# Performance work log

Hardware: AMD Instinct MI355X
Metric: run time of the kernel (lower is better)

The kernel has to match this reference:

```python
import jax, jax.numpy as jnp
import numpy as np

N, D, E = 100000, 128, 1600000


def setup_inputs() -> dict:
    key = jax.random.key(0)
    k1, k2, k3, k4, k5 = jax.random.split(key, 5)
    x = jax.random.normal(k1, (N, D), dtype=jnp.float32)
    edge_index = jax.random.randint(k2, (2, E), 0, N, dtype=jnp.int64)
    # xavier_uniform bound for [D, D]: sqrt(6/(D+D))
    bound = float(np.sqrt(6.0 / (D + D)))
    W_gcn = jax.random.uniform(k3, (D, D), jnp.float32, -bound, bound)
    b_gcn = jnp.zeros((D,), jnp.float32)  # GCNConv bias (default init zeros)
    # nn.Linear(bias=False) default init: uniform(-1/sqrt(fan_in), +)
    lb = float(1.0 / np.sqrt(D))
    W_ln = jax.random.uniform(k4, (D, D), jnp.float32, -lb, lb)  # [out, in]
    return {"x": x, "edge_index": edge_index, "W_gcn": W_gcn, "b_gcn": b_gcn, "W_ln": W_ln}


def gcn_conv(x, edge_index, W, b):
    n = x.shape[0]
    # add self loops
    loops = jnp.arange(n, dtype=edge_index.dtype)
    src = jnp.concatenate([edge_index[0], loops])
    dst = jnp.concatenate([edge_index[1], loops])
    h = x @ W  # [N, D] transform first (cheap), then propagate
    ones = jnp.ones(src.shape[0], dtype=x.dtype)
    deg = jax.ops.segment_sum(ones, dst, num_segments=n)  # >= 1 due to self loops
    dinv = jax.lax.rsqrt(deg)
    norm = dinv[src] * dinv[dst]  # [E+N]
    msgs = h[src] * norm[:, None]  # gather + scale
    agg = jax.ops.segment_sum(msgs, dst, num_segments=n)  # scatter-add
    return agg + b


def reference(x, edge_index, W_gcn, b_gcn, W_ln):
    out = gcn_conv(x, edge_index, W_gcn, b_gcn)
    out = jax.nn.relu(out)
    out = out @ W_ln.T  # Linear(bias=False): y = x W^T
    out = out + x       # residual
    return jax.nn.relu(out)
```

## Files before the change

kernel.cpp:

```cpp
#include <hip/hip_runtime.h>

#define DFEAT 128
#define CAP   32
#define PSH   9
#define PNODES (1 << PSH)
#define PMAX  1024
#define REGCAP 10240
#define SPILLMAX 4096
#define CHUNK 4096

__device__ __forceinline__ unsigned pack_bf16_2(float a, float b) {
    unsigned ua = __float_as_uint(a);
    unsigned ub = __float_as_uint(b);
    ua = (ua + 0x7FFFu + ((ua >> 16) & 1u)) >> 16;
    ub = (ub + 0x7FFFu + ((ub >> 16) & 1u)) >> 16;
    return ua | (ub << 16);
}

__global__ __launch_bounds__(256) void partA_kernel(const int* __restrict__ ei,
                                                    unsigned* __restrict__ rec,
                                                    int* __restrict__ gcur,
                                                    int2* __restrict__ spill,
                                                    int* __restrict__ spillcnt,
                                                    int E) {
    __shared__ int lhist[PMAX];
    int tid  = threadIdx.x;
    int base = blockIdx.x * CHUNK;
    int end  = min(base + CHUNK, E);
    for (int i = tid; i < PMAX; i += 256) lhist[i] = 0;
    __syncthreads();
    for (int e = base + tid; e < end; e += 256) {
        int dst = ei[E + e];
        atomicAdd(&lhist[dst >> PSH], 1);
    }
    __syncthreads();
    for (int p = tid; p < PMAX; p += 256) {
        int c = lhist[p];
        if (c > 0) lhist[p] = atomicAdd(&gcur[p], c);
    }
    __syncthreads();
    for (int e = base + tid; e < end; e += 256) {
        int src = ei[e];
        int dst = ei[E + e];
        int p   = dst >> PSH;
        int off = atomicAdd(&lhist[p], 1);
        if (off < REGCAP) {
            rec[(size_t)p * REGCAP + off] =
                ((unsigned)(dst & (PNODES - 1)) << 23) | (unsigned)src;
        } else {
            int sp = atomicAdd(spillcnt, 1);
            if (sp < SPILLMAX) spill[sp] = make_int2(dst, src);
        }
    }
}

__global__ __launch_bounds__(256) void partB_kernel(const unsigned* __restrict__ rec,
                                                    const int* __restrict__ gcur,
                                                    int* __restrict__ buf,
                                                    int* __restrict__ cnt,
                                                    float* __restrict__ dinv,
                                                    int2* __restrict__ spill,
                                                    int* __restrict__ spillcnt,
                                                    int n) {
    __shared__ int lcnt[PNODES];
    __shared__ int lbuf[PNODES * CAP];
    int tid   = threadIdx.x;
    int p     = blockIdx.x;
    int node0 = p << PSH;
    for (int i = tid; i < PNODES; i += 256) lcnt[i] = 0;
    __syncthreads();
    int total = gcur[p];
    if (total > REGCAP) total = REGCAP;
    const unsigned* r = rec + (size_t)p * REGCAP;
    for (int i = tid; i < total; i += 256) {
        unsigned v = r[i];
        int ldst = (int)(v >> 23);
        int src  = (int)(v & 0x7FFFFFu);
        int pos  = atomicAdd(&lcnt[ldst], 1);
        if (pos < CAP) lbuf[(ldst << 5) + pos] = src;
        else {
            int sp = atomicAdd(spillcnt, 1);
            if (sp < SPILLMAX) spill[sp] = make_int2(node0 + ldst, src);
        }
    }
    __syncthreads();
    int nn = min(PNODES, n - node0);
    if (nn <= 0) return;
    int vecs = (nn * CAP) >> 2;
    int4*       gb = (int4*)(buf + (size_t)node0 * CAP);
    const int4* lb = (const int4*)lbuf;
    for (int i = tid; i < vecs; i += 256) gb[i] = lb[i];
    for (int t = tid; t < nn; t += 256) {
        int c = lcnt[t];
        cnt[node0 + t]  = c;
        dinv[node0 + t] = rsqrtf((float)(c + 1));
    }
}

__global__ __launch_bounds__(512) void gemm1_kernel(const float* __restrict__ x,
                                                    const float* __restrict__ W,
                                                    const float* __restrict__ dinv,
                                                    unsigned* __restrict__ h, int n) {
    __shared__ float Wl[DFEAT * DFEAT];
    int tid = threadIdx.x;
#pragma unroll
    for (int it = 0; it < 8; ++it) {
        int idx = tid * 4 + it * 2048;
        *(float4*)(&Wl[idx]) = *(const float4*)(W + idx);
    }
    __syncthreads();

    int ty = tid >> 4;
    int tx = tid & 15;
    int row0 = blockIdx.x * 128 + ty * 4;
    int c0a = tx * 4, c0b = 64 + tx * 4;

    int rr[4];
#pragma unroll
    for (int i = 0; i < 4; i++) { int r = row0 + i; rr[i] = (r < n) ? r : (n - 1); }

    float acc[4][8];
#pragma unroll
    for (int i = 0; i < 4; i++)
#pragma unroll
        for (int j = 0; j < 8; j++) acc[i][j] = 0.f;

    for (int k = 0; k < DFEAT; k += 4) {
        float4 a[4];
#pragma unroll
        for (int i = 0; i < 4; i++)
            a[i] = *(const float4*)(x + (size_t)rr[i] * DFEAT + k);
#pragma unroll
        for (int kk = 0; kk < 4; kk++) {
            float4 w0 = *(const float4*)(&Wl[(k + kk) * DFEAT + c0a]);
            float4 w1 = *(const float4*)(&Wl[(k + kk) * DFEAT + c0b]);
#pragma unroll
            for (int i = 0; i < 4; i++) {
                float av = (kk == 0) ? a[i].x : (kk == 1) ? a[i].y : (kk == 2) ? a[i].z : a[i].w;
                acc[i][0] = fmaf(av, w0.x, acc[i][0]);
                acc[i][1] = fmaf(av, w0.y, acc[i][1]);
                acc[i][2] = fmaf(av, w0.z, acc[i][2]);
                acc[i][3] = fmaf(av, w0.w, acc[i][3]);
                acc[i][4] = fmaf(av, w1.x, acc[i][4]);
                acc[i][5] = fmaf(av, w1.y, acc[i][5]);
                acc[i][6] = fmaf(av, w1.z, acc[i][6]);
                acc[i][7] = fmaf(av, w1.w, acc[i][7]);
            }
        }
    }
#pragma unroll
    for (int i = 0; i < 4; i++) {
        int r = row0 + i;
        if (r < n) {
            float s = dinv[r];
            uint2 o0 = make_uint2(pack_bf16_2(acc[i][0] * s, acc[i][1] * s),
                                  pack_bf16_2(acc[i][2] * s, acc[i][3] * s));
            uint2 o1 = make_uint2(pack_bf16_2(acc[i][4] * s, acc[i][5] * s),
                                  pack_bf16_2(acc[i][6] * s, acc[i][7] * s));
            *(uint2*)(h + (size_t)r * 64 + tx * 2)      = o0;
            *(uint2*)(h + (size_t)r * 64 + 32 + tx * 2) = o1;
        }
    }
}

__global__ __launch_bounds__(256) void propagate_kernel(const unsigned* __restrict__ h,
                                                        const int* __restrict__ buf,
                                                        const int* __restrict__ cnt,
                                                        const float* __restrict__ dinv,
                                                        float* __restrict__ agg, int n) {
    int wave = (blockIdx.x * 256 + threadIdx.x) >> 6;
    int lane = threadIdx.x & 63;
    if (wave >= n) return;

    int c = cnt[wave];
    if (c > CAP) c = CAP;
    float di = dinv[wave];

    int mysrc = 0;
    if (lane < c) mysrc = buf[wave * CAP + lane];

    unsigned sv = h[(size_t)wave * 64 + lane];
    float ax = __uint_as_float(sv << 16);
    float ay = __uint_as_float(sv & 0xFFFF0000u);

    int k = 0;
    for (; k + 7 < c; k += 8) {
        int s[8];
#pragma unroll
        for (int j = 0; j < 8; j++) s[j] = __shfl(mysrc, k + j);
        unsigned v[8];
#pragma unroll
        for (int j = 0; j < 8; j++) v[j] = h[(size_t)s[j] * 64 + lane];
        float sx = 0.f, sy = 0.f;
#pragma unroll
        for (int j = 0; j < 8; j++) {
            sx += __uint_as_float(v[j] << 16);
            sy += __uint_as_float(v[j] & 0xFFFF0000u);
        }
        ax += sx;
        ay += sy;
    }
    for (; k < c; k++) {
        int sidx = __shfl(mysrc, k);
        unsigned v = h[(size_t)sidx * 64 + lane];
        ax += __uint_as_float(v << 16);
        ay += __uint_as_float(v & 0xFFFF0000u);
    }
    float2 acc = make_float2(ax * di, ay * di);
    ((float2*)agg)[(size_t)wave * 64 + lane] = acc;
}

__global__ __launch_bounds__(256) void spill_kernel(const unsigned* __restrict__ h,
                                                    const int2* __restrict__ spill,
                                                    const int* __restrict__ spillcnt,
                                                    const float* __restrict__ dinv,
                                                    float* __restrict__ agg) {
    int w = (blockIdx.x * 256 + threadIdx.x) >> 6;
    int lane = threadIdx.x & 63;
    int sc = *spillcnt;
    if (sc > SPILLMAX) sc = SPILLMAX;
    if (w >= sc) return;
    int2 e = spill[w];
    float di = dinv[e.x];
    unsigned v = h[(size_t)e.y * 64 + lane];
    atomicAdd(&agg[(size_t)e.x * DFEAT + 2 * lane],     __uint_as_float(v << 16) * di);
    atomicAdd(&agg[(size_t)e.x * DFEAT + 2 * lane + 1], __uint_as_float(v & 0xFFFF0000u) * di);
}

__device__ __forceinline__ int swz(int k, int c) { return c ^ (((k >> 2) & 7) << 2); }

__global__ __launch_bounds__(512) void gemm2_kernel(const float* __restrict__ agg,
                                                    const float* __restrict__ Wln,
                                                    const float* __restrict__ bias,
                                                    const float* __restrict__ x,
                                                    float* __restrict__ out, int n) {
    __shared__ float Wl[DFEAT * DFEAT];
    int tid = threadIdx.x;
#pragma unroll
    for (int it = 0; it < 8; ++it) {
        int idx = tid * 4 + it * 2048;
        float4 v = *(const float4*)(Wln + idx);
        int o  = idx >> 7;
        int ii = idx & 127;
        Wl[(ii + 0) * DFEAT + swz(ii + 0, o)] = v.x;
        Wl[(ii + 1) * DFEAT + swz(ii + 1, o)] = v.y;
        Wl[(ii + 2) * DFEAT + swz(ii + 2, o)] = v.z;
        Wl[(ii + 3) * DFEAT + swz(ii + 3, o)] = v.w;
    }
    __syncthreads();

    int ty = tid >> 4;
    int tx = tid & 15;
    int row0 = blockIdx.x * 128 + ty * 4;
    int c0a = tx * 4, c0b = 64 + tx * 4;

    int rr[4];
#pragma unroll
    for (int i = 0; i < 4; i++) { int r = row0 + i; rr[i] = (r < n) ? r : (n - 1); }

    float acc[4][8];
#pragma unroll
    for (int i = 0; i < 4; i++)
#pragma unroll
        for (int j = 0; j < 8; j++) acc[i][j] = 0.f;

    for (int k = 0; k < DFEAT; k += 4) {
        float4 bv = *(const float4*)(bias + k);
        float4 a[4];
#pragma unroll
        for (int i = 0; i < 4; i++) {
            float4 v = *(const float4*)(agg + (size_t)rr[i] * DFEAT + k);
            v.x = fmaxf(v.x + bv.x, 0.f);
            v.y = fmaxf(v.y + bv.y, 0.f);
            v.z = fmaxf(v.z + bv.z, 0.f);
            v.w = fmaxf(v.w + bv.w, 0.f);
            a[i] = v;
        }
#pragma unroll
        for (int kk = 0; kk < 4; kk++) {
            int krow = k + kk;
            float4 w0 = *(const float4*)(&Wl[krow * DFEAT + swz(krow, c0a)]);
            float4 w1 = *(const float4*)(&Wl[krow * DFEAT + swz(krow, c0b)]);
#pragma unroll
            for (int i = 0; i < 4; i++) {
                float av = (kk == 0) ? a[i].x : (kk == 1) ? a[i].y : (kk == 2) ? a[i].z : a[i].w;
                acc[i][0] = fmaf(av, w0.x, acc[i][0]);
                acc[i][1] = fmaf(av, w0.y, acc[i][1]);
                acc[i][2] = fmaf(av, w0.z, acc[i][2]);
                acc[i][3] = fmaf(av, w0.w, acc[i][3]);
                acc[i][4] = fmaf(av, w1.x, acc[i][4]);
                acc[i][5] = fmaf(av, w1.y, acc[i][5]);
                acc[i][6] = fmaf(av, w1.z, acc[i][6]);
                acc[i][7] = fmaf(av, w1.w, acc[i][7]);
            }
        }
    }
#pragma unroll
    for (int i = 0; i < 4; i++) {
        int r = row0 + i;
        if (r < n) {
            float4 x0 = *(const float4*)(x + (size_t)r * DFEAT + c0a);
            float4 x1 = *(const float4*)(x + (size_t)r * DFEAT + c0b);
            float4 o0 = make_float4(fmaxf(acc[i][0] + x0.x, 0.f), fmaxf(acc[i][1] + x0.y, 0.f),
                                    fmaxf(acc[i][2] + x0.z, 0.f), fmaxf(acc[i][3] + x0.w, 0.f));
            float4 o1 = make_float4(fmaxf(acc[i][4] + x1.x, 0.f), fmaxf(acc[i][5] + x1.y, 0.f),
                                    fmaxf(acc[i][6] + x1.z, 0.f), fmaxf(acc[i][7] + x1.w, 0.f));
            *(float4*)(out + (size_t)r * DFEAT + c0a) = o0;
            *(float4*)(out + (size_t)r * DFEAT + c0b) = o1;
        }
    }
}

extern "C" void kernel_launch(void* const* d_in, const int* in_sizes, int n_in,
                              void* d_out, int out_size, void* d_ws, size_t ws_size,
                              hipStream_t stream) {
    const float* x    = (const float*)d_in[0];
    const int*   ei   = (const int*)d_in[1];
    const float* Wg   = (const float*)d_in[2];
    const float* bg   = (const float*)d_in[3];
    const float* Wln  = (const float*)d_in[4];
    float*       out  = (float*)d_out;

    int n = in_sizes[0] / DFEAT;
    int E = in_sizes[1] / 2;
    int K = (n + PNODES - 1) >> PSH;

    size_t off = 0;
    auto take = [&](size_t bytes) {
        void* p = (char*)d_ws + off;
        off += (bytes + 255) & ~(size_t)255;
        return p;
    };
    int*      gcur  = (int*)take((size_t)PMAX * 4);
    int*      spc   = (int*)take(256);
    int*      cnt   = (int*)take((size_t)n * 4);
    float*    dinv  = (float*)take((size_t)n * 4);
    int2*     spill = (int2*)take((size_t)SPILLMAX * 8);
    unsigned* rec   = (unsigned*)take((size_t)K * REGCAP * 4);
    int*      buf   = (int*)take((size_t)n * CAP * 4);
    unsigned* h     = (unsigned*)take((size_t)n * 64 * 4);

    hipMemsetAsync(gcur, 0, (size_t)PMAX * 4, stream);
    hipMemsetAsync(spc, 0, 4, stream);
    partA_kernel<<<(E + CHUNK - 1) / CHUNK, 256, 0, stream>>>(ei, rec, gcur, spill, spc, E);
    partB_kernel<<<K, 256, 0, stream>>>(rec, gcur, buf, cnt, dinv, spill, spc, n);
    gemm1_kernel<<<(n + 127) / 128, 512, 0, stream>>>(x, Wg, dinv, h, n);
    propagate_kernel<<<(n + 3) / 4, 256, 0, stream>>>(h, buf, cnt, dinv, out, n);
    spill_kernel<<<SPILLMAX / 4, 256, 0, stream>>>(h, spill, spc, dinv, out);
    gemm2_kernel<<<(n + 127) / 128, 512, 0, stream>>>(out, Wln, bg, x, out, n);
}
```

Baseline: 326.0 us.

## Move both dense GEMMs to bf16 MFMA with split hi/lo precision emulation

```diff
diff --git a/kernel.cpp b/kernel.cpp
--- a/kernel.cpp
+++ b/kernel.cpp
@@ -8,13 +8,18 @@
 #define REGCAP 10240
 #define SPILLMAX 4096
 #define CHUNK 4096
-
+#define GROWS 192
+
+typedef __attribute__((ext_vector_type(8))) short bf16x8;
+typedef __attribute__((ext_vector_type(4))) float f32x4;
+
+__device__ __forceinline__ unsigned bf16_rtn(float x) {
+    unsigned u = __float_as_uint(x);
+    return (u + 0x7FFFu + ((u >> 16) & 1u)) >> 16;
+}
+__device__ __forceinline__ float bf16f(unsigned b) { return __uint_as_float(b << 16); }
 __device__ __forceinline__ unsigned pack_bf16_2(float a, float b) {
-    unsigned ua = __float_as_uint(a);
-    unsigned ub = __float_as_uint(b);
-    ua = (ua + 0x7FFFu + ((ua >> 16) & 1u)) >> 16;
-    ub = (ub + 0x7FFFu + ((ub >> 16) & 1u)) >> 16;
-    return ua | (ub << 16);
+    return bf16_rtn(a) | (bf16_rtn(b) << 16);
 }
 
 __global__ __launch_bounds__(256) void partA_kernel(const int* __restrict__ ei,
@@ -97,68 +102,93 @@
     }
 }
 
-__global__ __launch_bounds__(512) void gemm1_kernel(const float* __restrict__ x,
+__global__ __launch_bounds__(256) void gemm1_kernel(const float* __restrict__ x,
                                                     const float* __restrict__ W,
                                                     const float* __restrict__ dinv,
                                                     unsigned* __restrict__ h, int n) {
-    __shared__ float Wl[DFEAT * DFEAT];
+    __shared__ unsigned short Wh[DFEAT * DFEAT];
+    __shared__ unsigned short Wl[DFEAT * DFEAT];
     int tid = threadIdx.x;
-#pragma unroll
-    for (int it = 0; it < 8; ++it) {
-        int idx = tid * 4 + it * 2048;
-        *(float4*)(&Wl[idx]) = *(const float4*)(W + idx);
-    }
-    __syncthreads();
-
-    int ty = tid >> 4;
-    int tx = tid & 15;
-    int row0 = blockIdx.x * 128 + ty * 4;
-    int c0a = tx * 4, c0b = 64 + tx * 4;
-
-    int rr[4];
-#pragma unroll
-    for (int i = 0; i < 4; i++) { int r = row0 + i; rr[i] = (r < n) ? r : (n - 1); }
-
-    float acc[4][8];
-#pragma unroll
-    for (int i = 0; i < 4; i++)
-#pragma unroll
-        for (int j = 0; j < 8; j++) acc[i][j] = 0.f;
-
-    for (int k = 0; k < DFEAT; k += 4) {
-        float4 a[4];
-#pragma unroll
-        for (int i = 0; i < 4; i++)
-            a[i] = *(const float4*)(x + (size_t)rr[i] * DFEAT + k);
-#pragma unroll
-        for (int kk = 0; kk < 4; kk++) {
-            float4 w0 = *(const float4*)(&Wl[(k + kk) * DFEAT + c0a]);
-            float4 w1 = *(const float4*)(&Wl[(k + kk) * DFEAT + c0b]);
-#pragma unroll
-            for (int i = 0; i < 4; i++) {
-                float av = (kk == 0) ? a[i].x : (kk == 1) ? a[i].y : (kk == 2) ? a[i].z : a[i].w;
-                acc[i][0] = fmaf(av, w0.x, acc[i][0]);
-                acc[i][1] = fmaf(av, w0.y, acc[i][1]);
-                acc[i][2] = fmaf(av, w0.z, acc[i][2]);
-                acc[i][3] = fmaf(av, w0.w, acc[i][3]);
-                acc[i][4] = fmaf(av, w1.x, acc[i][4]);
-                acc[i][5] = fmaf(av, w1.y, acc[i][5]);
-                acc[i][6] = fmaf(av, w1.z, acc[i][6]);
-                acc[i][7] = fmaf(av, w1.w, acc[i][7]);
-            }
-        }
-    }
-#pragma unroll
-    for (int i = 0; i < 4; i++) {
-        int r = row0 + i;
-        if (r < n) {
-            float s = dinv[r];
-            uint2 o0 = make_uint2(pack_bf16_2(acc[i][0] * s, acc[i][1] * s),
-                                  pack_bf16_2(acc[i][2] * s, acc[i][3] * s));
-            uint2 o1 = make_uint2(pack_bf16_2(acc[i][4] * s, acc[i][5] * s),
-                                  pack_bf16_2(acc[i][6] * s, acc[i][7] * s));
-            *(uint2*)(h + (size_t)r * 64 + tx * 2)      = o0;
-            *(uint2*)(h + (size_t)r * 64 + 32 + tx * 2) = o1;
+    {
+        int c = tid & 127, kh = tid >> 7;
+        for (int kc = 0; kc < 64; kc += 8) {
+            int k0 = kh * 64 + kc;
+            float w8[8];
+#pragma unroll
+            for (int j = 0; j < 8; j++) w8[j] = W[(size_t)(k0 + j) * DFEAT + c];
+            bf16x8 hv, lv;
+#pragma unroll
+            for (int j = 0; j < 8; j++) {
+                unsigned hb = bf16_rtn(w8[j]);
+                hv[j] = (short)hb;
+                lv[j] = (short)bf16_rtn(w8[j] - bf16f(hb));
+            }
+            int byte = (c << 8) + ((k0 * 2) ^ ((c & 7) << 4));
+            *(bf16x8*)((char*)Wh + byte) = hv;
+            *(bf16x8*)((char*)Wl + byte) = lv;
+        }
+    }
+    __syncthreads();
+
+    int w    = tid >> 6;
+    int l    = tid & 63;
+    int row0 = blockIdx.x * GROWS + w * 48;
+    int lr   = l & 15;
+    int lq   = l >> 4;
+
+    f32x4 acc[3][8];
+#pragma unroll
+    for (int s = 0; s < 3; s++)
+#pragma unroll
+        for (int ct = 0; ct < 8; ct++) acc[s][ct] = (f32x4){0.f, 0.f, 0.f, 0.f};
+
+    for (int kt = 0; kt < 4; kt++) {
+        int k0 = kt * 32 + lq * 8;
+        bf16x8 ah[3], al[3];
+#pragma unroll
+        for (int s = 0; s < 3; s++) {
+            int rw = row0 + s * 16 + lr;
+            int rc = (rw < n) ? rw : (n - 1);
+            const float* xp = x + (size_t)rc * DFEAT + k0;
+            float v[8];
+            *(float4*)(v)     = *(const float4*)(xp);
+            *(float4*)(v + 4) = *(const float4*)(xp + 4);
+#pragma unroll
+            for (int j = 0; j < 8; j++) {
+                unsigned hb = bf16_rtn(v[j]);
+                ah[s][j] = (short)hb;
+                al[s][j] = (short)bf16_rtn(v[j] - bf16f(hb));
+            }
+        }
+#pragma unroll
+        for (int ct = 0; ct < 8; ct++) {
+            int brow = ct * 16 + lr;
+            int byte = (brow << 8) + ((k0 * 2) ^ ((brow & 7) << 4));
+            bf16x8 bh = *(const bf16x8*)((const char*)Wh + byte);
+            bf16x8 bl = *(const bf16x8*)((const char*)Wl + byte);
+#pragma unroll
+            for (int s = 0; s < 3; s++) {
+                acc[s][ct] = __builtin_amdgcn_mfma_f32_16x16x32_bf16(ah[s], bh, acc[s][ct], 0, 0, 0);
+                acc[s][ct] = __builtin_amdgcn_mfma_f32_16x16x32_bf16(al[s], bh, acc[s][ct], 0, 0, 0);
+                acc[s][ct] = __builtin_amdgcn_mfma_f32_16x16x32_bf16(ah[s], bl, acc[s][ct], 0, 0, 0);
+            }
+        }
+    }
+
+#pragma unroll
+    for (int s = 0; s < 3; s++) {
+#pragma unroll
+        for (int r = 0; r < 4; r++) {
+            int rw = row0 + s * 16 + lq * 4 + r;
+            int rc = (rw < n) ? rw : (n - 1);
+            float di = dinv[rc];
+#pragma unroll
+            for (int ct = 0; ct < 8; ct++) {
+                float v = acc[s][ct][r] * di;
+                float o = __shfl_xor(v, 1);
+                if (((l & 1) == 0) && rw < n)
+                    h[(size_t)rw * 64 + ct * 8 + (lr >> 1)] = pack_bf16_2(v, o);
+            }
         }
     }
 }
@@ -206,8 +236,7 @@
         ax += __uint_as_float(v << 16);
         ay += __uint_as_float(v & 0xFFFF0000u);
     }
-    float2 acc = make_float2(ax * di, ay * di);
-    ((float2*)agg)[(size_t)wave * 64 + lane] = acc;
+    ((float2*)agg)[(size_t)wave * 64 + lane] = make_float2(ax * di, ay * di);
 }
 
 __global__ __launch_bounds__(256) void spill_kernel(const unsigned* __restrict__ h,
@@ -227,86 +256,97 @@
     atomicAdd(&agg[(size_t)e.x * DFEAT + 2 * lane + 1], __uint_as_float(v & 0xFFFF0000u) * di);
 }
 
-__device__ __forceinline__ int swz(int k, int c) { return c ^ (((k >> 2) & 7) << 2); }
-
-__global__ __launch_bounds__(512) void gemm2_kernel(const float* __restrict__ agg,
+__global__ __launch_bounds__(256) void gemm2_kernel(const float* __restrict__ agg,
                                                     const float* __restrict__ Wln,
                                                     const float* __restrict__ bias,
                                                     const float* __restrict__ x,
                                                     float* __restrict__ out, int n) {
-    __shared__ float Wl[DFEAT * DFEAT];
+    __shared__ unsigned short Bh[DFEAT * DFEAT];
+    __shared__ unsigned short Bl[DFEAT * DFEAT];
     int tid = threadIdx.x;
-#pragma unroll
-    for (int it = 0; it < 8; ++it) {
-        int idx = tid * 4 + it * 2048;
-        float4 v = *(const float4*)(Wln + idx);
-        int o  = idx >> 7;
-        int ii = idx & 127;
-        Wl[(ii + 0) * DFEAT + swz(ii + 0, o)] = v.x;
-        Wl[(ii + 1) * DFEAT + swz(ii + 1, o)] = v.y;
-        Wl[(ii + 2) * DFEAT + swz(ii + 2, o)] = v.z;
-        Wl[(ii + 3) * DFEAT + swz(ii + 3, o)] = v.w;
-    }
-    __syncthreads();
-
-    int ty = tid >> 4;
-    int tx = tid & 15;
-    int row0 = blockIdx.x * 128 + ty * 4;
-    int c0a = tx * 4, c0b = 64 + tx * 4;
-
-    int rr[4];
-#pragma unroll
-    for (int i = 0; i < 4; i++) { int r = row0 + i; rr[i] = (r < n) ? r : (n - 1); }
-
-    float acc[4][8];
-#pragma unroll
-    for (int i = 0; i < 4; i++)
-#pragma unroll
-        for (int j = 0; j < 8; j++) acc[i][j] = 0.f;
-
-    for (int k = 0; k < DFEAT; k += 4) {
-        float4 bv = *(const float4*)(bias + k);
-        float4 a[4];
-#pragma unroll
-        for (int i = 0; i < 4; i++) {
-            float4 v = *(const float4*)(agg + (size_t)rr[i] * DFEAT + k);
-            v.x = fmaxf(v.x + bv.x, 0.f);
-            v.y = fmaxf(v.y + bv.y, 0.f);
-            v.z = fmaxf(v.z + bv.z, 0.f);
-            v.w = fmaxf(v.w + bv.w, 0.f);
-            a[i] = v;
-        }
-#pragma unroll
-        for (int kk = 0; kk < 4; kk++) {
-            int krow = k + kk;
-            float4 w0 = *(const float4*)(&Wl[krow * DFEAT + swz(krow, c0a)]);
-            float4 w1 = *(const float4*)(&Wl[krow * DFEAT + swz(krow, c0b)]);
-#pragma unroll
-            for (int i = 0; i < 4; i++) {
-                float av = (kk == 0) ? a[i].x : (kk == 1) ? a[i].y : (kk == 2) ? a[i].z : a[i].w;
-                acc[i][0] = fmaf(av, w0.x, acc[i][0]);
-                acc[i][1] = fmaf(av, w0.y, acc[i][1]);
-                acc[i][2] = fmaf(av, w0.z, acc[i][2]);
-                acc[i][3] = fmaf(av, w0.w, acc[i][3]);
-                acc[i][4] = fmaf(av, w1.x, acc[i][4]);
-                acc[i][5] = fmaf(av, w1.y, acc[i][5]);
-                acc[i][6] = fmaf(av, w1.z, acc[i][6]);
-                acc[i][7] = fmaf(av, w1.w, acc[i][7]);
-            }
-        }
-    }
-#pragma unroll
-    for (int i = 0; i < 4; i++) {
-        int r = row0 + i;
-        if (r < n) {
-            float4 x0 = *(const float4*)(x + (size_t)r * DFEAT + c0a);
-            float4 x1 = *(const float4*)(x + (size_t)r * DFEAT + c0b);
-            float4 o0 = make_float4(fmaxf(acc[i][0] + x0.x, 0.f), fmaxf(acc[i][1] + x0.y, 0.f),
-                                    fmaxf(acc[i][2] + x0.z, 0.f), fmaxf(acc[i][3] + x0.w, 0.f));
-            float4 o1 = make_float4(fmaxf(acc[i][4] + x1.x, 0.f), fmaxf(acc[i][5] + x1.y, 0.f),
-                                    fmaxf(acc[i][6] + x1.z, 0.f), fmaxf(acc[i][7] + x1.w, 0.f));
-            *(float4*)(out + (size_t)r * DFEAT + c0a) = o0;
-            *(float4*)(out + (size_t)r * DFEAT + c0b) = o1;
+    {
+        int o = tid & 127, kh = tid >> 7;
+        for (int kc = 0; kc < 64; kc += 8) {
+            int k0 = kh * 64 + kc;
+            float w8[8];
+            *(float4*)(w8)     = *(const float4*)(Wln + (size_t)o * DFEAT + k0);
+            *(float4*)(w8 + 4) = *(const float4*)(Wln + (size_t)o * DFEAT + k0 + 4);
+            bf16x8 hv, lv;
+#pragma unroll
+            for (int j = 0; j < 8; j++) {
+                unsigned hb = bf16_rtn(w8[j]);
+                hv[j] = (short)hb;
+                lv[j] = (short)bf16_rtn(w8[j] - bf16f(hb));
+            }
+            int byte = (o << 8) + ((k0 * 2) ^ ((o & 7) << 4));
+            *(bf16x8*)((char*)Bh + byte) = hv;
+            *(bf16x8*)((char*)Bl + byte) = lv;
+        }
+    }
+    __syncthreads();
+
+    int w    = tid >> 6;
+    int l    = tid & 63;
+    int row0 = blockIdx.x * GROWS + w * 48;
+    int lr   = l & 15;
+    int lq   = l >> 4;
+
+    f32x4 acc[3][8];
+#pragma unroll
+    for (int s = 0; s < 3; s++)
+#pragma unroll
+        for (int ct = 0; ct < 8; ct++) acc[s][ct] = (f32x4){0.f, 0.f, 0.f, 0.f};
+
+    for (int kt = 0; kt < 4; kt++) {
+        int k0 = kt * 32 + lq * 8;
+        float bb[8];
+        *(float4*)(bb)     = *(const float4*)(bias + k0);
+        *(float4*)(bb + 4) = *(const float4*)(bias + k0 + 4);
+        bf16x8 ah[3], al[3];
+#pragma unroll
+        for (int s = 0; s < 3; s++) {
+            int rw = row0 + s * 16 + lr;
+            int rc = (rw < n) ? rw : (n - 1);
+            const float* ap = agg + (size_t)rc * DFEAT + k0;
+            float v[8];
+            *(float4*)(v)     = *(const float4*)(ap);
+            *(float4*)(v + 4) = *(const float4*)(ap + 4);
+#pragma unroll
+            for (int j = 0; j < 8; j++) {
+                float a = fmaxf(v[j] + bb[j], 0.f);
+                unsigned hb = bf16_rtn(a);
+                ah[s][j] = (short)hb;
+                al[s][j] = (short)bf16_rtn(a - bf16f(hb));
+            }
+        }
+#pragma unroll
+        for (int ct = 0; ct < 8; ct++) {
+            int brow = ct * 16 + lr;
+            int byte = (brow << 8) + ((k0 * 2) ^ ((brow & 7) << 4));
+            bf16x8 bh = *(const bf16x8*)((const char*)Bh + byte);
+            bf16x8 bl = *(const bf16x8*)((const char*)Bl + byte);
+#pragma unroll
+            for (int s = 0; s < 3; s++) {
+                acc[s][ct] = __builtin_amdgcn_mfma_f32_16x16x32_bf16(ah[s], bh, acc[s][ct], 0, 0, 0);
+                acc[s][ct] = __builtin_amdgcn_mfma_f32_16x16x32_bf16(al[s], bh, acc[s][ct], 0, 0, 0);
+                acc[s][ct] = __builtin_amdgcn_mfma_f32_16x16x32_bf16(ah[s], bl, acc[s][ct], 0, 0, 0);
+            }
+        }
+    }
+
+#pragma unroll
+    for (int s = 0; s < 3; s++) {
+#pragma unroll
+        for (int r = 0; r < 4; r++) {
+            int rw = row0 + s * 16 + lq * 4 + r;
+            if (rw < n) {
+#pragma unroll
+                for (int ct = 0; ct < 8; ct++) {
+                    int col = ct * 16 + lr;
+                    float v = acc[s][ct][r] + x[(size_t)rw * DFEAT + col];
+                    out[(size_t)rw * DFEAT + col] = fmaxf(v, 0.f);
+                }
+            }
         }
     }
 }
@@ -340,12 +380,14 @@
     int*      buf   = (int*)take((size_t)n * CAP * 4);
     unsigned* h     = (unsigned*)take((size_t)n * 64 * 4);
 
+    int gblocks = (n + GROWS - 1) / GROWS;
+
     hipMemsetAsync(gcur, 0, (size_t)PMAX * 4, stream);
     hipMemsetAsync(spc, 0, 4, stream);
     partA_kernel<<<(E + CHUNK - 1) / CHUNK, 256, 0, stream>>>(ei, rec, gcur, spill, spc, E);
     partB_kernel<<<K, 256, 0, stream>>>(rec, gcur, buf, cnt, dinv, spill, spc, n);
-    gemm1_kernel<<<(n + 127) / 128, 512, 0, stream>>>(x, Wg, dinv, h, n);
+    gemm1_kernel<<<gblocks, 256, 0, stream>>>(x, Wg, dinv, h, n);
     propagate_kernel<<<(n + 3) / 4, 256, 0, stream>>>(h, buf, cnt, dinv, out, n);
     spill_kernel<<<SPILLMAX / 4, 256, 0, stream>>>(h, spill, spc, dinv, out);
-    gemm2_kernel<<<(n + 127) / 128, 512, 0, stream>>>(out, Wln, bg, x, out, n);
-}
+    gemm2_kernel<<<gblocks, 256, 0, stream>>>(out, Wln, bg, x, out, n);
+}
```

Result: faster. 281.7 us (-13.6%).
